# Performance work log

Hardware: AMD Instinct MI355X
Metric: run time of the kernel (lower is better)

Reference implementation:

```python
import jax, jax.numpy as jnp
import numpy as np

ALPHA = 0.2
N_ENT, N_TYP, N_REL, E = 100000, 1000, 200, 500000
D = 64          # nfeat1 = nfeat2 = nhid1 = nhid2 = relation_dim
NHEADS = 2      # forced by the tuple-unpack in the original forward


def _xavier(key, shape):
    fan_out, fan_in = shape[0], shape[-1]
    lim = 1.414 * np.sqrt(6.0 / (fan_in + fan_out))
    return jax.random.uniform(key, shape, jnp.float32, -lim, lim)


def setup_inputs() -> dict:
    key = jax.random.key(0)
    ks = jax.random.split(key, 32)
    inp = {
        "entity_embeddings": jax.random.normal(ks[0], (N_ENT, D), jnp.float32),
        "type_embed": jax.random.normal(ks[1], (N_TYP, D), jnp.float32),
        "relation_embed": jax.random.normal(ks[2], (N_REL, D), jnp.float32),
        "edge_list": jax.random.randint(ks[3], (2, E), 0, N_TYP),  # row0=src entity, row1=dst type; both in-range
        "edge_type": jax.random.randint(ks[4], (E,), 0, N_REL),
        "edge_embed": jax.random.normal(ks[5], (E, D), jnp.float32),
    }
    Din = 3 * D  # cat(x1[src], x2[dst], edge_embed)
    i = 6
    for h in range(NHEADS):
        inp[f"a_e{h}"] = _xavier(ks[i], (D, Din)); i += 1   # entity-side attention proj
        inp[f"v_e{h}"] = _xavier(ks[i], (1, D))[0]; i += 1  # entity-side score vector
        inp[f"a_t{h}"] = _xavier(ks[i], (D, Din)); i += 1   # type-side attention proj
        inp[f"v_t{h}"] = _xavier(ks[i], (1, D))[0]; i += 1
    Ho = NHEADS * D       # 128
    Dout = 3 * Ho         # out layer input cat dim
    inp["a_eo"] = _xavier(ks[i], (Ho, Dout)); i += 1
    inp["v_eo"] = _xavier(ks[i], (1, Ho))[0]; i += 1
    inp["a_to"] = _xavier(ks[i], (Ho, Dout)); i += 1
    inp["v_to"] = _xavier(ks[i], (1, Ho))[0]; i += 1
    inp["W"] = _xavier(ks[i], (D, Ho))  # relation_dim -> nheads*nhid1
    return inp


def _gat_e2t(x1, x2, src, dst, e, a_e, v_e, a_t, v_t, concat):
    """Bipartite sparse GAT layer (KBGAT-style, e2t variant).
    Message m = a @ cat(x1[src], x2[dst], edge_embed); score = exp(-leaky_relu(v . m));
    softmax-normalized scatter-aggregate to entity nodes (by src) and type nodes (by dst)."""
    d1, d2 = x1.shape[1], x2.shape[1]

    def agg(a, v, seg, nseg):
        a1, a2, a3 = a[:, :d1], a[:, d1:d1 + d2], a[:, d1 + d2:]
        # project nodes first, then gather (avoids materializing [E, 3d] cat)
        m = (x1 @ a1.T)[src] + (x2 @ a2.T)[dst] + e @ a3.T     # [E, h]
        s = jnp.exp(-jax.nn.leaky_relu(m @ v, ALPHA))          # [E] unnormalized attention
        num = jax.ops.segment_sum(m * s[:, None], seg, num_segments=nseg)
        den = jax.ops.segment_sum(s, seg, num_segments=nseg)
        h = num / jnp.where(den == 0, 1.0, den)[:, None]
        return jax.nn.elu(h) if concat else h

    h_e = agg(a_e, v_e, src, x1.shape[0])
    h_t = agg(a_t, v_t, dst, x2.shape[0])
    return h_e, h_t


def reference(entity_embeddings, type_embed, relation_embed, edge_list, edge_type, edge_embed,
              a_e0, v_e0, a_t0, v_t0, a_e1, v_e1, a_t1, v_t1,
              a_eo, v_eo, a_to, v_to, W):
    src, dst = edge_list[0], edge_list[1]
    # two attention heads (concat=True -> elu inside)
    h0e, h0t = _gat_e2t(entity_embeddings, type_embed, src, dst, edge_embed, a_e0, v_e0, a_t0, v_t0, True)
    h1e, h1t = _gat_e2t(entity_embeddings, type_embed, src, dst, edge_embed, a_e1, v_e1, a_t1, v_t1, True)
    x1 = jnp.concatenate([h0e, h1e], axis=1)  # [N_ENT, 2*nhid1]
    x2 = jnp.concatenate([h0t, h1t], axis=1)  # [N_TYP, 2*nhid2]
    # dropout is identity at inference
    out_rel = relation_embed @ W              # [N_REL, nheads*nhid1]
    e2 = out_rel[edge_type]                   # per-edge relation embedding
    o1, o2 = _gat_e2t(x1, x2, src, dst, e2, a_eo, v_eo, a_to, v_to, False)
    return jax.nn.elu(o1), jax.nn.elu(o2), out_rel
```

## Files before the change

### kernel.cpp

```cpp
#include <hip/hip_runtime.h>

#define ALPHA 0.2f
#define NT 1000
#define NRELC 200
#define NE 500000
#define N_ENT 100000
#define CH 2048
#define G 245

static constexpr size_t I_STARTS_SRC = 0;
static constexpr size_t I_STARTS_DST = 1001;
static constexpr size_t I_COLSUM     = 2002;
static constexpr size_t I_HIST2      = 4002;
static constexpr size_t I_BASE2      = 494002;
static constexpr size_t I_AB_SRC     = 984002;
static constexpr size_t I_AB_DST     = 1984002;

static constexpr size_t F_U1 = 2984004;
static constexpr size_t F_U2 = F_U1 + 768;
static constexpr size_t F_L1 = F_U2 + 768;
static constexpr size_t F_X1 = F_L1 + 4*130000;
static constexpr size_t F_X2 = F_X1 + 128000;
static constexpr size_t F_OR = F_X2 + 128000;
static constexpr size_t F_L2 = F_OR + 25600;
static constexpr size_t S2F = 283800;
static constexpr size_t WS_FLOATS = F_L2 + 2*S2F;

static constexpr size_t OUT_O2  = 12800000;
static constexpr size_t OUT_REL = 12928000;

__device__ __forceinline__ float eluf(float x) { return x > 0.f ? x : expm1f(x); }
__device__ __forceinline__ float scoref(float slin) {
  return expf(slin > 0.f ? -slin : -ALPHA * slin);
}

__global__ __launch_bounds__(256) void k_hist2(const int* __restrict__ src,
                                               const int* __restrict__ dst,
                                               int* __restrict__ ip) {
  __shared__ int h[NT];
  int bid = blockIdx.x;
  int side = bid >= G;
  int blk = bid - side * G;
  const int* keys = side ? dst : src;
  int j0 = blk * CH;
  int n = min(CH, NE - j0);
  for (int i = threadIdx.x; i < NT; i += 256) h[i] = 0;
  __syncthreads();
  for (int k = threadIdx.x; k < n; k += 256) atomicAdd(&h[keys[j0 + k]], 1);
  __syncthreads();
  int* row = ip + I_HIST2 + (size_t)(side * G + blk) * NT;
  for (int b = threadIdx.x; b < NT; b += 256) row[b] = h[b];
}

__global__ void k_colsum(int* __restrict__ ip) {
  int t = blockIdx.x * 256 + threadIdx.x;
  if (t >= 2 * NT) return;
  int side = t / NT, bin = t - side * NT;
  int s = 0;
  for (int blk = 0; blk < G; ++blk)
    s += ip[I_HIST2 + (size_t)(side * G + blk) * NT + bin];
  ip[I_COLSUM + t] = s;
}

__global__ void k_scan2b(int* __restrict__ ip) {
  __shared__ int buf[1024];
  int t = threadIdx.x;
  for (int side = 0; side < 2; ++side) {
    int v = (t < NT) ? ip[I_COLSUM + side * NT + t] : 0;
    buf[t] = v;
    __syncthreads();
    for (int off = 1; off < 1024; off <<= 1) {
      int x = (t >= off) ? buf[t - off] : 0;
      __syncthreads();
      buf[t] += x;
      __syncthreads();
    }
    int* st = ip + (side ? I_STARTS_DST : I_STARTS_SRC);
    if (t < NT) st[t] = buf[t] - v;
    if (t == NT - 1) st[NT] = buf[t];
    __syncthreads();
  }
}

__global__ void k_bases(int* __restrict__ ip) {
  int t = blockIdx.x * 256 + threadIdx.x;
  if (t >= 2 * NT) return;
  int side = t / NT, bin = t - side * NT;
  int run = ip[(side ? I_STARTS_DST : I_STARTS_SRC) + bin];
  for (int blk = 0; blk < G; ++blk) {
    size_t idx = I_HIST2 + (size_t)(side * G + blk) * NT + bin;
    int c = ip[idx];
    ip[idx + (I_BASE2 - I_HIST2)] = run;
    run += c;
  }
}

__global__ __launch_bounds__(256) void k_binscat(const int* __restrict__ src,
                                                 const int* __restrict__ dst,
                                                 const int* __restrict__ et,
                                                 int* __restrict__ ip) {
  __shared__ int2 bufs[CH];
  __shared__ int loff[1024];
  __shared__ int lcur[1024];
  __shared__ int gbase[1024];
  __shared__ int psum[256];
  int bid = blockIdx.x;
  int side = bid >= G;
  int blk = bid - side * G;
  const int* keys = side ? dst : src;
  const int* oths = side ? src : dst;
  int j0 = blk * CH;
  int n = min(CH, NE - j0);
  int t = threadIdx.x;

  for (int i = t; i < 1024; i += 256) lcur[i] = 0;
  __syncthreads();
  for (int k = t; k < n; k += 256) atomicAdd(&lcur[keys[j0 + k]], 1);
  __syncthreads();
  int c0 = lcur[4*t], c1 = lcur[4*t+1], c2 = lcur[4*t+2], c3 = lcur[4*t+3];
  int s = c0 + c1 + c2 + c3;
  psum[t] = s;
  __syncthreads();
  for (int off = 1; off < 256; off <<= 1) {
    int x = (t >= off) ? psum[t - off] : 0;
    __syncthreads();
    psum[t] += x;
    __syncthreads();
  }
  int base = psum[t] - s;
  loff[4*t]   = base;
  loff[4*t+1] = base + c0;
  loff[4*t+2] = base + c0 + c1;
  loff[4*t+3] = base + c0 + c1 + c2;
  lcur[4*t]   = loff[4*t];
  lcur[4*t+1] = loff[4*t+1];
  lcur[4*t+2] = loff[4*t+2];
  lcur[4*t+3] = loff[4*t+3];
  const int* brow = ip + I_BASE2 + (size_t)(side * G + blk) * NT;
  for (int b = t; b < NT; b += 256) gbase[b] = brow[b];
  __syncthreads();
  for (int k = t; k < n; k += 256) {
    int j = j0 + k;
    int b = keys[j];
    int pos = atomicAdd(&lcur[b], 1);
    bufs[pos] = make_int2(j | (b << 19), oths[j] | (et[j] << 16));
  }
  __syncthreads();
  int2* out = reinterpret_cast<int2*>(ip + (side ? I_AB_DST : I_AB_SRC));
  for (int k = t; k < n; k += 256) {
    int2 q = bufs[k];
    int b = q.x >> 19;
    int posg = gbase[b] + (k - loff[b]);
    out[posg] = make_int2(q.x & 0x7FFFF, q.y);
  }
}

__global__ void k_prep_u(const float* aE0, const float* vE0, const float* aT0, const float* vT0,
                         const float* aE1, const float* vE1, const float* aT1, const float* vT1,
                         const float* aEo, const float* vEo, const float* aTo, const float* vTo,
                         float* ws) {
  int t = blockIdx.x * blockDim.x + threadIdx.x;
  if (t < 768) {
    int c = t / 192, rem = t - c*192;
    int p = rem >> 6, k = rem & 63;
    const float* a = (c==0)?aE0:(c==1)?aT0:(c==2)?aE1:aT1;
    const float* v = (c==0)?vE0:(c==1)?vT0:(c==2)?vE1:vT1;
    float s = 0.f;
    for (int o = 0; o < 64; ++o) s += a[o*192 + p*64 + k] * v[o];
    ws[F_U1 + (size_t)(c*3+p)*64 + k] = s;
  } else if (t < 1536) {
    int tt = t - 768;
    int c = tt / 384, rem = tt - c*384;
    int p = rem >> 7, k = rem & 127;
    const float* a = c ? aTo : aEo;
    const float* v = c ? vTo : vEo;
    float s = 0.f;
    for (int o = 0; o < 128; ++o) s += a[o*384 + p*128 + k] * v[o];
    ws[F_U2 + (size_t)(c*3+p)*128 + k] = s;
  }
}

__global__ __launch_bounds__(256) void k_l1_proj(const float* Ent, const float* Typ,
                                                 const float* aE0, const float* aT0,
                                                 const float* aE1, const float* aT1,
                                                 float* ws) {
  int bid = blockIdx.x;
  int t = threadIdx.x;
  if (bid < 504) {
    __shared__ float xs[16][64];
    int c = bid / 126, rem = bid - c*126;
    int table = rem / 63, tile = rem - table*63;
    int i0 = tile * 16;
    const float* a = (c==0)?aE0:(c==1)?aT0:(c==2)?aE1:aT1;
    const float* x = table ? Typ : Ent;
    float* outb = ws + F_L1 + (size_t)c*130000 + (table ? 64000 : 0);
    for (int idx = t; idx < 1024; idx += 256) {
      int r = idx >> 6, k = idx & 63;
      int i = i0 + r;
      xs[r][k] = (i < NT) ? x[(size_t)i*64 + k] : 0.f;
    }
    __syncthreads();
    int o = t & 63, grp = t >> 6;
    const float* arow = a + o*192 + table*64;
    float acc0 = 0.f, acc1 = 0.f, acc2 = 0.f, acc3 = 0.f;
    #pragma unroll 8
    for (int k = 0; k < 64; ++k) {
      float av = arow[k];
      acc0 += xs[grp*4+0][k] * av;
      acc1 += xs[grp*4+1][k] * av;
      acc2 += xs[grp*4+2][k] * av;
      acc3 += xs[grp*4+3][k] * av;
    }
    int ib = i0 + grp*4;
    if (ib + 0 < NT) outb[(size_t)(ib+0)*64 + o] = acc0;
    if (ib + 1 < NT) outb[(size_t)(ib+1)*64 + o] = acc1;
    if (ib + 2 < NT) outb[(size_t)(ib+2)*64 + o] = acc2;
    if (ib + 3 < NT) outb[(size_t)(ib+3)*64 + o] = acc3;
  } else {
    int idx = (bid - 504) * 256 + t;
    if (idx >= 8000) return;
    int c = idx / 2000, rem = idx - c*2000;
    float* base = ws + F_L1 + (size_t)c * 130000;
    if (rem < 1000) {
      const float* x = Ent + (size_t)rem*64;
      const float* u = ws + F_U1 + (size_t)(c*3)*64;
      float s = 0.f;
      #pragma unroll
      for (int k = 0; k < 64; ++k) s += x[k]*u[k];
      base[128000 + rem] = s;
    } else {
      int i = rem - 1000;
      const float* x = Typ + (size_t)i*64;
      const float* u = ws + F_U1 + (size_t)(c*3+1)*64;
      float s = 0.f;
      #pragma unroll
      for (int k = 0; k < 64; ++k) s += x[k]*u[k];
      base[129000 + i] = s;
    }
  }
}

__global__ __launch_bounds__(256) void k_l1_acc(const float* __restrict__ Eemb,
                                                const float* aE0, const float* aT0,
                                                const float* aE1, const float* aT1,
                                                const int* __restrict__ ip,
                                                float* __restrict__ ws) {
  __shared__ float smem[4434];
  float* TlB   = smem;
  float* cOth0 = smem + 2000;
  float* cOth1 = smem + 3000;
  float* accRf = smem + 2000;
  float* accEf = smem + 4048;
  float* redf  = smem + 4176;
  float* denf  = smem + 4432;

  int side = blockIdx.x >= NT;
  int g = blockIdx.x - side * NT;
  int t = threadIdx.x;
  int sub = t & 15, slot = t >> 4;
  int c0 = side, c1 = side + 2;

  size_t othOff = side ? 128000 : 129000;
  size_t ownOff = side ? 129000 : 128000;
  for (int i = t; i < NT; i += 256) {
    TlB[i] = 0.f; TlB[1000 + i] = 0.f;
    cOth0[i] = ws[F_L1 + (size_t)c0*130000 + othOff + i];
    cOth1[i] = ws[F_L1 + (size_t)c1*130000 + othOff + i];
  }
  if (t < 2) denf[t] = 0.f;
  float ownA = ws[F_L1 + (size_t)c0*130000 + ownOff + g];
  float ownB = ws[F_L1 + (size_t)c1*130000 + ownOff + g];
  float4 w3A = reinterpret_cast<const float4*>(ws + F_U1 + (size_t)(c0*3+2)*64)[sub];
  float4 w3B = reinterpret_cast<const float4*>(ws + F_U1 + (size_t)(c1*3+2)*64)[sub];
  __syncthreads();

  int start = ip[(side ? I_STARTS_DST : I_STARTS_SRC) + g];
  int end   = ip[(side ? I_STARTS_DST : I_STARTS_SRC) + g + 1];
  const int2* ab = reinterpret_cast<const int2*>(ip + (side ? I_AB_DST : I_AB_SRC));
  const float4* EV = reinterpret_cast<const float4*>(Eemb);

  float4 acc0 = make_float4(0.f,0.f,0.f,0.f);
  float4 acc1 = make_float4(0.f,0.f,0.f,0.f);
  float d0 = 0.f, d1 = 0.f;

  int p = start + slot;
  for (; p + 48 < end; p += 64) {
    int2 q0 = ab[p], q1 = ab[p+16], q2 = ab[p+32], q3 = ab[p+48];
    float4 e0 = EV[(size_t)q0.x*16 + sub];
    float4 e1 = EV[(size_t)q1.x*16 + sub];
    float4 e2 = EV[(size_t)q2.x*16 + sub];
    float4 e3 = EV[(size_t)q3.x*16 + sub];
    float rA0 = e0.x*w3A.x + e0.y*w3A.y + e0.z*w3A.z + e0.w*w3A.w;
    float rB0 = e0.x*w3B.x + e0.y*w3B.y + e0.z*w3B.z + e0.w*w3B.w;
    float rA1 = e1.x*w3A.x + e1.y*w3A.y + e1.z*w3A.z + e1.w*w3A.w;
    float rB1 = e1.x*w3B.x + e1.y*w3B.y + e1.z*w3B.z + e1.w*w3B.w;
    float rA2 = e2.x*w3A.x + e2.y*w3A.y + e2.z*w3A.z + e2.w*w3A.w;
    float rB2 = e2.x*w3B.x + e2.y*w3B.y + e2.z*w3B.z + e2.w*w3B.w;
    float rA3 = e3.x*w3A.x + e3.y*w3A.y + e3.z*w3A.z + e3.w*w3A.w;
    float rB3 = e3.x*w3B.x + e3.y*w3B.y + e3.z*w3B.z + e3.w*w3B.w;
    #pragma unroll
    for (int sh = 1; sh < 16; sh <<= 1) {
      rA0 += __shfl_xor(rA0, sh, 16); rB0 += __shfl_xor(rB0, sh, 16);
      rA1 += __shfl_xor(rA1, sh, 16); rB1 += __shfl_xor(rB1, sh, 16);
      rA2 += __shfl_xor(rA2, sh, 16); rB2 += __shfl_xor(rB2, sh, 16);
      rA3 += __shfl_xor(rA3, sh, 16); rB3 += __shfl_xor(rB3, sh, 16);
    }
    int o0 = q0.y & 0xFFFF, o1 = q1.y & 0xFFFF, o2 = q2.y & 0xFFFF, o3 = q3.y & 0xFFFF;
    float sA0 = scoref(ownA + cOth0[o0] + rA0);
    float sB0 = scoref(ownB + cOth1[o0] + rB0);
    float sA1 = scoref(ownA + cOth0[o1] + rA1);
    float sB1 = scoref(ownB + cOth1[o1] + rB1);
    float sA2 = scoref(ownA + cOth0[o2] + rA2);
    float sB2 = scoref(ownB + cOth1[o2] + rB2);
    float sA3 = scoref(ownA + cOth0[o3] + rA3);
    float sB3 = scoref(ownB + cOth1[o3] + rB3);
    acc0.x += sA0*e0.x + sA1*e1.x + sA2*e2.x + sA3*e3.x;
    acc0.y += sA0*e0.y + sA1*e1.y + sA2*e2.y + sA3*e3.y;
    acc0.z += sA0*e0.z + sA1*e1.z + sA2*e2.z + sA3*e3.z;
    acc0.w += sA0*e0.w + sA1*e1.w + sA2*e2.w + sA3*e3.w;
    acc1.x += sB0*e0.x + sB1*e1.x + sB2*e2.x + sB3*e3.x;
    acc1.y += sB0*e0.y + sB1*e1.y + sB2*e2.y + sB3*e3.y;
    acc1.z += sB0*e0.z + sB1*e1.z + sB2*e2.z + sB3*e3.z;
    acc1.w += sB0*e0.w + sB1*e1.w + sB2*e2.w + sB3*e3.w;
    if (sub == 0) {
      atomicAdd(&TlB[o0], sA0); atomicAdd(&TlB[1000+o0], sB0);
      atomicAdd(&TlB[o1], sA1); atomicAdd(&TlB[1000+o1], sB1);
      atomicAdd(&TlB[o2], sA2); atomicAdd(&TlB[1000+o2], sB2);
      atomicAdd(&TlB[o3], sA3); atomicAdd(&TlB[1000+o3], sB3);
      d0 += sA0 + sA1 + sA2 + sA3;
      d1 += sB0 + sB1 + sB2 + sB3;
    }
  }
  for (; p < end; p += 16) {
    int2 q = ab[p];
    float4 ev = EV[(size_t)q.x*16 + sub];
    float rA = ev.x*w3A.x + ev.y*w3A.y + ev.z*w3A.z + ev.w*w3A.w;
    float rB = ev.x*w3B.x + ev.y*w3B.y + ev.z*w3B.z + ev.w*w3B.w;
    #pragma unroll
    for (int sh = 1; sh < 16; sh <<= 1) {
      rA += __shfl_xor(rA, sh, 16);
      rB += __shfl_xor(rB, sh, 16);
    }
    int oth = q.y & 0xFFFF;
    float sA = scoref(ownA + cOth0[oth] + rA);
    float sB = scoref(ownB + cOth1[oth] + rB);
    acc0.x += sA*ev.x; acc0.y += sA*ev.y; acc0.z += sA*ev.z; acc0.w += sA*ev.w;
    acc1.x += sB*ev.x; acc1.y += sB*ev.y; acc1.z += sB*ev.z; acc1.w += sB*ev.w;
    if (sub == 0) {
      atomicAdd(&TlB[oth], sA);
      atomicAdd(&TlB[1000+oth], sB);
      d0 += sA; d1 += sB;
    }
  }
  __syncthreads();
  *reinterpret_cast<float4*>(&accRf[slot*64 + sub*4])        = acc0;
  *reinterpret_cast<float4*>(&accRf[1024 + slot*64 + sub*4]) = acc1;
  if (sub == 0) { atomicAdd(&denf[0], d0); atomicAdd(&denf[1], d1); }
  __syncthreads();
  if (t < 128) {
    int ci = t >> 6, o = t & 63;
    float s = 0.f;
    #pragma unroll
    for (int sl = 0; sl < 16; ++sl) s += accRf[ci*1024 + sl*64 + o];
    accEf[ci*64 + o] = s;
  }
  __syncthreads();

  int o = t & 63, part = t >> 6;
  size_t othPOff = side ? 0 : 64000;
  size_t ownPOff = side ? 64000 : 0;
  #pragma unroll
  for (int ci = 0; ci < 2; ++ci) {
    int c = side + 2*ci;
    const float* Pc = ws + F_L1 + (size_t)c * 130000;
    const float* Poth = Pc + othPOff;
    float sum = 0.f;
    for (int dd = part*250; dd < part*250 + 250; ++dd)
      sum += TlB[ci*1000 + dd] * Poth[(size_t)dd*64 + o];
    redf[t] = sum;
    __syncthreads();
    if (part == 0) {
      sum = redf[o] + redf[64+o] + redf[128+o] + redf[192+o];
      const float* a = (c==0)?aE0:(c==1)?aT0:(c==2)?aE1:aT1;
      const float* a3 = a + o*192 + 128;
      float acc = 0.f;
      #pragma unroll
      for (int k = 0; k < 64; ++k) acc += accEf[ci*64 + k]*a3[k];
      float den = denf[ci];
      float own = Pc[ownPOff + (size_t)g*64 + o];
      float num = sum + acc + den*own;
      float h = num / (den == 0.f ? 1.f : den);
      float* dst = ws + (side ? F_X2 : F_X1);
      dst[(size_t)g*128 + ci*64 + o] = eluf(h);
    }
    __syncthreads();
  }
}

__global__ void k_relW(const float* Rel, const float* W, float* ws, float* dout) {
  int t = blockIdx.x * blockDim.x + threadIdx.x;
  if (t >= NRELC*128) return;
  int r = t >> 7, o = t & 127;
  const float* x = Rel + (size_t)r*64;
  float s = 0.f;
  #pragma unroll
  for (int k = 0; k < 64; ++k) s += x[k] * W[(size_t)k*128 + o];
  ws[F_OR + t] = s;
  dout[OUT_REL + t] = s;
}

__global__ __launch_bounds__(256) void k_l2_proj(const float* aEo, const float* aTo,
                                                 float* ws) {
  int bid = blockIdx.x;
  int t = threadIdx.x;
  const float* x1 = ws + F_X1;
  const float* x2 = ws + F_X2;
  const float* orel = ws + F_OR;
  if (bid < 278) {
    __shared__ float xs[16][128];
    int c = bid / 139, rem = bid - c*139;
    const float* a = c ? aTo : aEo;
    float* cb = ws + F_L2 + (size_t)c * S2F;
    const float* x; int part, tile, nrows; float* outb;
    if (rem < 63)       { x = x1;   part = 0; tile = rem;       nrows = NT;    outb = cb; }
    else if (rem < 126) { x = x2;   part = 1; tile = rem - 63;  nrows = NT;    outb = cb + 128000; }
    else                { x = orel; part = 2; tile = rem - 126; nrows = NRELC; outb = cb + 256000; }
    int i0 = tile * 16;
    for (int idx = t; idx < 2048; idx += 256) {
      int r = idx >> 7, k = idx & 127;
      int i = i0 + r;
      xs[r][k] = (i < nrows) ? x[(size_t)i*128 + k] : 0.f;
    }
    __syncthreads();
    int o = t & 127, grp = t >> 7;
    const float* arow = a + (size_t)o*384 + part*128;
    float acc[8] = {0.f,0.f,0.f,0.f,0.f,0.f,0.f,0.f};
    #pragma unroll 4
    for (int k = 0; k < 128; ++k) {
      float av = arow[k];
      #pragma unroll
      for (int r = 0; r < 8; ++r)
        acc[r] += xs[grp*8+r][k] * av;
    }
    int ib = i0 + grp*8;
    #pragma unroll
    for (int r = 0; r < 8; ++r)
      if (ib + r < nrows) outb[(size_t)(ib+r)*128 + o] = acc[r];
  } else {
    int idx = (bid - 278) * 256 + t;
    if (idx >= 4400) return;
    int c = idx / 2200, rem = idx - c*2200;
    float* base = ws + F_L2 + (size_t)c * S2F;
    if (rem < 1000) {
      const float* u = ws + F_U2 + (size_t)(c*3)*128;
      const float* x = x1 + (size_t)rem*128;
      float s = 0.f;
      for (int k = 0; k < 128; ++k) s += x[k]*u[k];
      base[281600 + rem] = s;
    } else if (rem < 2000) {
      int i = rem - 1000;
      const float* u = ws + F_U2 + (size_t)(c*3+1)*128;
      const float* x = x2 + (size_t)i*128;
      float s = 0.f;
      for (int k = 0; k < 128; ++k) s += x[k]*u[k];
      base[282600 + i] = s;
    } else {
      int r = rem - 2000;
      const float* u = ws + F_U2 + (size_t)(c*3+2)*128;
      const float* x = orel + (size_t)r*128;
      float s = 0.f;
      for (int k = 0; k < 128; ++k) s += x[k]*u[k];
      base[283600 + r] = s;
    }
  }
}

__global__ __launch_bounds__(256) void k_l2_seg(const int* __restrict__ ip,
                                                float* __restrict__ ws,
                                                float* __restrict__ dout) {
  __shared__ float Tl[2][NT];
  __shared__ float Ul[2][NRELC];
  __shared__ float cOthL[NT];
  __shared__ float cRelL[NRELC];
  __shared__ float red[2][256];
  __shared__ float denl[2];

  int c = blockIdx.x >= 500;
  int gp = blockIdx.x - c * 500;
  int g0 = gp * 2;
  int t = threadIdx.x;
  float* base = ws + F_L2 + (size_t)c * S2F;

  size_t othOff = c ? 281600 : 282600;
  size_t ownOff = c ? 282600 : 281600;
  for (int i = t; i < NT; i += 256) { Tl[0][i] = 0.f; Tl[1][i] = 0.f; cOthL[i] = base[othOff + i]; }
  for (int i = t; i < NRELC; i += 256) { Ul[0][i] = 0.f; Ul[1][i] = 0.f; cRelL[i] = base[283600 + i]; }
  if (t < 2) denl[t] = 0.f;
  float own0 = base[ownOff + g0];
  float own1 = base[ownOff + g0 + 1];
  __syncthreads();

  const int* st = ip + (c ? I_STARTS_DST : I_STARTS_SRC);
  int s0 = st[g0], split = st[g0 + 1], e1 = st[g0 + 2];
  const int2* ab = reinterpret_cast<const int2*>(ip + (c ? I_AB_DST : I_AB_SRC));

  float d0 = 0.f, d1 = 0.f;
  for (int p = s0 + t; p < e1; p += 256) {
    int2 q = ab[p];
    int oth = q.y & 0xFFFF;
    int r = q.y >> 16;
    int ls = p >= split;
    float sv = scoref((ls ? own1 : own0) + cOthL[oth] + cRelL[r]);
    atomicAdd(&Tl[ls][oth], sv);
    atomicAdd(&Ul[ls][r], sv);
    if (ls) d1 += sv; else d0 += sv;
  }
  atomicAdd(&denl[0], d0);
  atomicAdd(&denl[1], d1);
  __syncthreads();

  int o = t & 127, part = t >> 7;
  const float* Qoth = base + (c ? 0 : 128000);
  const float* R3 = base + 256000;
  float sum0 = 0.f, sum1 = 0.f;
  for (int dd = part*500; dd < part*500 + 500; ++dd) {
    float qv = Qoth[(size_t)dd*128 + o];
    sum0 += Tl[0][dd] * qv;
    sum1 += Tl[1][dd] * qv;
  }
  for (int rr = part*100; rr < part*100 + 100; ++rr) {
    float qv = R3[(size_t)rr*128 + o];
    sum0 += Ul[0][rr] * qv;
    sum1 += Ul[1][rr] * qv;
  }
  red[0][t] = sum0;
  red[1][t] = sum1;
  __syncthreads();
  int li = part;
  float den = denl[li];
  float sum = red[li][o] + red[li][128 + o];
  int gw = g0 + li;
  float ownQ = base[(c ? 128000 : 0) + (size_t)gw*128 + o];
  float num = sum + den * ownQ;
  float h = num / (den == 0.f ? 1.f : den);
  size_t off = c ? (OUT_O2 + (size_t)gw*128 + o) : ((size_t)gw*128 + o);
  dout[off] = eluf(h);
}

extern "C" void kernel_launch(void* const* d_in, const int* in_sizes, int n_in,
                              void* d_out, int out_size, void* d_ws, size_t ws_size,
                              hipStream_t stream) {
  (void)in_sizes; (void)n_in;
  const float* Ent = (const float*)d_in[0];
  const float* Typ = (const float*)d_in[1];
  const float* Rel = (const float*)d_in[2];
  const int*   edge = (const int*)d_in[3];
  const int*   etyp = (const int*)d_in[4];
  const float* Eemb = (const float*)d_in[5];
  const float* aE0 = (const float*)d_in[6];
  const float* vE0 = (const float*)d_in[7];
  const float* aT0 = (const float*)d_in[8];
  const float* vT0 = (const float*)d_in[9];
  const float* aE1 = (const float*)d_in[10];
  const float* vE1 = (const float*)d_in[11];
  const float* aT1 = (const float*)d_in[12];
  const float* vT1 = (const float*)d_in[13];
  const float* aEo = (const float*)d_in[14];
  const float* vEo = (const float*)d_in[15];
  const float* aTo = (const float*)d_in[16];
  const float* vTo = (const float*)d_in[17];
  const float* W   = (const float*)d_in[18];
  float* ws  = (float*)d_ws;
  int*   ip  = (int*)d_ws;
  float* out = (float*)d_out;
  const int* srcA = edge;
  const int* dstA = edge + NE;

  if (ws_size < WS_FLOATS * sizeof(float)) return;

  hipMemsetAsync(d_out, 0, (size_t)out_size * sizeof(float), stream);

  k_hist2  <<<2*G, 256, 0, stream>>>(srcA, dstA, ip);
  k_colsum <<<8, 256, 0, stream>>>(ip);
  k_scan2b <<<1, 1024, 0, stream>>>(ip);
  k_bases  <<<8, 256, 0, stream>>>(ip);
  k_binscat<<<2*G, 256, 0, stream>>>(srcA, dstA, etyp, ip);
  k_prep_u <<<6, 256, 0, stream>>>(aE0,vE0,aT0,vT0,aE1,vE1,aT1,vT1,aEo,vEo,aTo,vTo,ws);
  k_l1_proj<<<536, 256, 0, stream>>>(Ent, Typ, aE0, aT0, aE1, aT1, ws);
  k_l1_acc <<<2000, 256, 0, stream>>>(Eemb, aE0, aT0, aE1, aT1, ip, ws);
  k_relW   <<<100, 256, 0, stream>>>(Rel, W, ws, out);
  k_l2_proj<<<296, 256, 0, stream>>>(aEo, aTo, ws);
  k_l2_seg <<<1000, 256, 0, stream>>>(ip, ws, out);
}
```

Measured before the change: 253.1 us.

## Embed per-edge other-side score terms in binned edge records

The edge binning kernel now runs after the layer-1 projections and writes 16-byte records that also carry the two precomputed other-side score contributions. The layer-1 accumulate kernel then reads these from the record instead of staging 1000-entry tables in shared memory. Its accumulator reduction is split into two passes so the shared-memory footprint shrinks, which may raise occupancy. In exchange, the edge-record arrays double in size, so layer 2, which also reads them, moves more bytes per edge.

```diff
diff --git a/kernel.cpp b/kernel.cpp
--- a/kernel.cpp
+++ b/kernel.cpp
@@ -13,10 +13,10 @@
 static constexpr size_t I_COLSUM     = 2002;
 static constexpr size_t I_HIST2      = 4002;
 static constexpr size_t I_BASE2      = 494002;
-static constexpr size_t I_AB_SRC     = 984002;
-static constexpr size_t I_AB_DST     = 1984002;
-
-static constexpr size_t F_U1 = 2984004;
+static constexpr size_t I_AB_SRC     = 984004;
+static constexpr size_t I_AB_DST     = 2984004;
+
+static constexpr size_t F_U1 = 4984004;
 static constexpr size_t F_U2 = F_U1 + 768;
 static constexpr size_t F_L1 = F_U2 + 768;
 static constexpr size_t F_X1 = F_L1 + 4*130000;
@@ -92,66 +92,6 @@
     int c = ip[idx];
     ip[idx + (I_BASE2 - I_HIST2)] = run;
     run += c;
-  }
-}
-
-__global__ __launch_bounds__(256) void k_binscat(const int* __restrict__ src,
-                                                 const int* __restrict__ dst,
-                                                 const int* __restrict__ et,
-                                                 int* __restrict__ ip) {
-  __shared__ int2 bufs[CH];
-  __shared__ int loff[1024];
-  __shared__ int lcur[1024];
-  __shared__ int gbase[1024];
-  __shared__ int psum[256];
-  int bid = blockIdx.x;
-  int side = bid >= G;
-  int blk = bid - side * G;
-  const int* keys = side ? dst : src;
-  const int* oths = side ? src : dst;
-  int j0 = blk * CH;
-  int n = min(CH, NE - j0);
-  int t = threadIdx.x;
-
-  for (int i = t; i < 1024; i += 256) lcur[i] = 0;
-  __syncthreads();
-  for (int k = t; k < n; k += 256) atomicAdd(&lcur[keys[j0 + k]], 1);
-  __syncthreads();
-  int c0 = lcur[4*t], c1 = lcur[4*t+1], c2 = lcur[4*t+2], c3 = lcur[4*t+3];
-  int s = c0 + c1 + c2 + c3;
-  psum[t] = s;
-  __syncthreads();
-  for (int off = 1; off < 256; off <<= 1) {
-    int x = (t >= off) ? psum[t - off] : 0;
-    __syncthreads();
-    psum[t] += x;
-    __syncthreads();
-  }
-  int base = psum[t] - s;
-  loff[4*t]   = base;
-  loff[4*t+1] = base + c0;
-  loff[4*t+2] = base + c0 + c1;
-  loff[4*t+3] = base + c0 + c1 + c2;
-  lcur[4*t]   = loff[4*t];
-  lcur[4*t+1] = loff[4*t+1];
-  lcur[4*t+2] = loff[4*t+2];
-  lcur[4*t+3] = loff[4*t+3];
-  const int* brow = ip + I_BASE2 + (size_t)(side * G + blk) * NT;
-  for (int b = t; b < NT; b += 256) gbase[b] = brow[b];
-  __syncthreads();
-  for (int k = t; k < n; k += 256) {
-    int j = j0 + k;
-    int b = keys[j];
-    int pos = atomicAdd(&lcur[b], 1);
-    bufs[pos] = make_int2(j | (b << 19), oths[j] | (et[j] << 16));
-  }
-  __syncthreads();
-  int2* out = reinterpret_cast<int2*>(ip + (side ? I_AB_DST : I_AB_SRC));
-  for (int k = t; k < n; k += 256) {
-    int2 q = bufs[k];
-    int b = q.x >> 19;
-    int posg = gbase[b] + (k - loff[b]);
-    out[posg] = make_int2(q.x & 0x7FFFF, q.y);
   }
 }
 
@@ -240,19 +180,83 @@
   }
 }
 
+__global__ __launch_bounds__(256) void k_binscat(const int* __restrict__ src,
+                                                 const int* __restrict__ dst,
+                                                 const int* __restrict__ et,
+                                                 int* __restrict__ ip,
+                                                 const float* __restrict__ ws) {
+  __shared__ int2 bufs[CH];
+  __shared__ int loff[1024];
+  __shared__ int lcur[1024];
+  __shared__ int gbase[1024];
+  __shared__ int psum[256];
+  int bid = blockIdx.x;
+  int side = bid >= G;
+  int blk = bid - side * G;
+  const int* keys = side ? dst : src;
+  const int* oths = side ? src : dst;
+  int j0 = blk * CH;
+  int n = min(CH, NE - j0);
+  int t = threadIdx.x;
+
+  for (int i = t; i < 1024; i += 256) lcur[i] = 0;
+  __syncthreads();
+  for (int k = t; k < n; k += 256) atomicAdd(&lcur[keys[j0 + k]], 1);
+  __syncthreads();
+  int c0 = lcur[4*t], c1 = lcur[4*t+1], c2 = lcur[4*t+2], c3 = lcur[4*t+3];
+  int s = c0 + c1 + c2 + c3;
+  psum[t] = s;
+  __syncthreads();
+  for (int off = 1; off < 256; off <<= 1) {
+    int x = (t >= off) ? psum[t - off] : 0;
+    __syncthreads();
+    psum[t] += x;
+    __syncthreads();
+  }
+  int base = psum[t] - s;
+  loff[4*t]   = base;
+  loff[4*t+1] = base + c0;
+  loff[4*t+2] = base + c0 + c1;
+  loff[4*t+3] = base + c0 + c1 + c2;
+  lcur[4*t]   = loff[4*t];
+  lcur[4*t+1] = loff[4*t+1];
+  lcur[4*t+2] = loff[4*t+2];
+  lcur[4*t+3] = loff[4*t+3];
+  const int* brow = ip + I_BASE2 + (size_t)(side * G + blk) * NT;
+  for (int b = t; b < NT; b += 256) gbase[b] = brow[b];
+  __syncthreads();
+  for (int k = t; k < n; k += 256) {
+    int j = j0 + k;
+    int b = keys[j];
+    int pos = atomicAdd(&lcur[b], 1);
+    bufs[pos] = make_int2(j | (b << 19), oths[j] | (et[j] << 16));
+  }
+  __syncthreads();
+  size_t othOff = side ? 128000 : 129000;
+  const float* cT0 = ws + F_L1 + (size_t)(side    )*130000 + othOff;
+  const float* cT1 = ws + F_L1 + (size_t)(side + 2)*130000 + othOff;
+  int4* out4 = reinterpret_cast<int4*>(ip + (side ? I_AB_DST : I_AB_SRC));
+  for (int k = t; k < n; k += 256) {
+    int2 q = bufs[k];
+    int b = q.x >> 19;
+    int posg = gbase[b] + (k - loff[b]);
+    int oth = q.y & 0xFFFF;
+    out4[posg] = make_int4(q.x & 0x7FFFF, q.y,
+                           __float_as_int(cT0[oth]), __float_as_int(cT1[oth]));
+  }
+}
+
 __global__ __launch_bounds__(256) void k_l1_acc(const float* __restrict__ Eemb,
                                                 const float* aE0, const float* aT0,
                                                 const float* aE1, const float* aT1,
                                                 const int* __restrict__ ip,
                                                 float* __restrict__ ws) {
-  __shared__ float smem[4434];
+  __shared__ float smem[3154];
   float* TlB   = smem;
-  float* cOth0 = smem + 2000;
-  float* cOth1 = smem + 3000;
   float* accRf = smem + 2000;
-  float* accEf = smem + 4048;
-  float* redf  = smem + 4176;
-  float* denf  = smem + 4432;
+  float* accEf = smem + 3024;
+  float* denf  = smem + 3152;
+  float* redf  = smem + 2000;
 
   int side = blockIdx.x >= NT;
   int g = blockIdx.x - side * NT;
@@ -260,13 +264,8 @@
   int sub = t & 15, slot = t >> 4;
   int c0 = side, c1 = side + 2;
 
-  size_t othOff = side ? 128000 : 129000;
   size_t ownOff = side ? 129000 : 128000;
-  for (int i = t; i < NT; i += 256) {
-    TlB[i] = 0.f; TlB[1000 + i] = 0.f;
-    cOth0[i] = ws[F_L1 + (size_t)c0*130000 + othOff + i];
-    cOth1[i] = ws[F_L1 + (size_t)c1*130000 + othOff + i];
-  }
+  for (int i = t; i < NT; i += 256) { TlB[i] = 0.f; TlB[1000 + i] = 0.f; }
   if (t < 2) denf[t] = 0.f;
   float ownA = ws[F_L1 + (size_t)c0*130000 + ownOff + g];
   float ownB = ws[F_L1 + (size_t)c1*130000 + ownOff + g];
@@ -276,7 +275,7 @@
 
   int start = ip[(side ? I_STARTS_DST : I_STARTS_SRC) + g];
   int end   = ip[(side ? I_STARTS_DST : I_STARTS_SRC) + g + 1];
-  const int2* ab = reinterpret_cast<const int2*>(ip + (side ? I_AB_DST : I_AB_SRC));
+  const int4* ab = reinterpret_cast<const int4*>(ip + (side ? I_AB_DST : I_AB_SRC));
   const float4* EV = reinterpret_cast<const float4*>(Eemb);
 
   float4 acc0 = make_float4(0.f,0.f,0.f,0.f);
@@ -285,7 +284,7 @@
 
   int p = start + slot;
   for (; p + 48 < end; p += 64) {
-    int2 q0 = ab[p], q1 = ab[p+16], q2 = ab[p+32], q3 = ab[p+48];
+    int4 q0 = ab[p], q1 = ab[p+16], q2 = ab[p+32], q3 = ab[p+48];
     float4 e0 = EV[(size_t)q0.x*16 + sub];
     float4 e1 = EV[(size_t)q1.x*16 + sub];
     float4 e2 = EV[(size_t)q2.x*16 + sub];
@@ -306,14 +305,14 @@
       rA3 += __shfl_xor(rA3, sh, 16); rB3 += __shfl_xor(rB3, sh, 16);
     }
     int o0 = q0.y & 0xFFFF, o1 = q1.y & 0xFFFF, o2 = q2.y & 0xFFFF, o3 = q3.y & 0xFFFF;
-    float sA0 = scoref(ownA + cOth0[o0] + rA0);
-    float sB0 = scoref(ownB + cOth1[o0] + rB0);
-    float sA1 = scoref(ownA + cOth0[o1] + rA1);
-    float sB1 = scoref(ownB + cOth1[o1] + rB1);
-    float sA2 = scoref(ownA + cOth0[o2] + rA2);
-    float sB2 = scoref(ownB + cOth1[o2] + rB2);
-    float sA3 = scoref(ownA + cOth0[o3] + rA3);
-    float sB3 = scoref(ownB + cOth1[o3] + rB3);
+    float sA0 = scoref(ownA + __int_as_float(q0.z) + rA0);
+    float sB0 = scoref(ownB + __int_as_float(q0.w) + rB0);
+    float sA1 = scoref(ownA + __int_as_float(q1.z) + rA1);
+    float sB1 = scoref(ownB + __int_as_float(q1.w) + rB1);
+    float sA2 = scoref(ownA + __int_as_float(q2.z) + rA2);
+    float sB2 = scoref(ownB + __int_as_float(q2.w) + rB2);
+    float sA3 = scoref(ownA + __int_as_float(q3.z) + rA3);
+    float sB3 = scoref(ownB + __int_as_float(q3.w) + rB3);
     acc0.x += sA0*e0.x + sA1*e1.x + sA2*e2.x + sA3*e3.x;
     acc0.y += sA0*e0.y + sA1*e1.y + sA2*e2.y + sA3*e3.y;
     acc0.z += sA0*e0.z + sA1*e1.z + sA2*e2.z + sA3*e3.z;
@@ -332,7 +331,7 @@
     }
   }
   for (; p < end; p += 16) {
-    int2 q = ab[p];
+    int4 q = ab[p];
     float4 ev = EV[(size_t)q.x*16 + sub];
     float rA = ev.x*w3A.x + ev.y*w3A.y + ev.z*w3A.z + ev.w*w3A.w;
     float rB = ev.x*w3B.x + ev.y*w3B.y + ev.z*w3B.z + ev.w*w3B.w;
@@ -342,8 +341,8 @@
       rB += __shfl_xor(rB, sh, 16);
     }
     int oth = q.y & 0xFFFF;
-    float sA = scoref(ownA + cOth0[oth] + rA);
-    float sB = scoref(ownB + cOth1[oth] + rB);
+    float sA = scoref(ownA + __int_as_float(q.z) + rA);
+    float sB = scoref(ownB + __int_as_float(q.w) + rB);
     acc0.x += sA*ev.x; acc0.y += sA*ev.y; acc0.z += sA*ev.z; acc0.w += sA*ev.w;
     acc1.x += sB*ev.x; acc1.y += sB*ev.y; acc1.z += sB*ev.z; acc1.w += sB*ev.w;
     if (sub == 0) {
@@ -352,17 +351,24 @@
       d0 += sA; d1 += sB;
     }
   }
-  __syncthreads();
-  *reinterpret_cast<float4*>(&accRf[slot*64 + sub*4])        = acc0;
-  *reinterpret_cast<float4*>(&accRf[1024 + slot*64 + sub*4]) = acc1;
   if (sub == 0) { atomicAdd(&denf[0], d0); atomicAdd(&denf[1], d1); }
   __syncthreads();
-  if (t < 128) {
-    int ci = t >> 6, o = t & 63;
+  *reinterpret_cast<float4*>(&accRf[slot*64 + sub*4]) = acc0;
+  __syncthreads();
+  if (t < 64) {
     float s = 0.f;
     #pragma unroll
-    for (int sl = 0; sl < 16; ++sl) s += accRf[ci*1024 + sl*64 + o];
-    accEf[ci*64 + o] = s;
+    for (int sl = 0; sl < 16; ++sl) s += accRf[sl*64 + t];
+    accEf[t] = s;
+  }
+  __syncthreads();
+  *reinterpret_cast<float4*>(&accRf[slot*64 + sub*4]) = acc1;
+  __syncthreads();
+  if (t < 64) {
+    float s = 0.f;
+    #pragma unroll
+    for (int sl = 0; sl < 16; ++sl) s += accRf[sl*64 + t];
+    accEf[64 + t] = s;
   }
   __syncthreads();
 
@@ -502,11 +508,11 @@
 
   const int* st = ip + (c ? I_STARTS_DST : I_STARTS_SRC);
   int s0 = st[g0], split = st[g0 + 1], e1 = st[g0 + 2];
-  const int2* ab = reinterpret_cast<const int2*>(ip + (c ? I_AB_DST : I_AB_SRC));
+  const int4* ab = reinterpret_cast<const int4*>(ip + (c ? I_AB_DST : I_AB_SRC));
 
   float d0 = 0.f, d1 = 0.f;
   for (int p = s0 + t; p < e1; p += 256) {
-    int2 q = ab[p];
+    int4 q = ab[p];
     int oth = q.y & 0xFFFF;
     int r = q.y >> 16;
     int ls = p >= split;
@@ -584,9 +590,9 @@
   k_colsum <<<8, 256, 0, stream>>>(ip);
   k_scan2b <<<1, 1024, 0, stream>>>(ip);
   k_bases  <<<8, 256, 0, stream>>>(ip);
-  k_binscat<<<2*G, 256, 0, stream>>>(srcA, dstA, etyp, ip);
   k_prep_u <<<6, 256, 0, stream>>>(aE0,vE0,aT0,vT0,aE1,vE1,aT1,vT1,aEo,vEo,aTo,vTo,ws);
   k_l1_proj<<<536, 256, 0, stream>>>(Ent, Typ, aE0, aT0, aE1, aT1, ws);
+  k_binscat<<<2*G, 256, 0, stream>>>(srcA, dstA, etyp, ip, ws);
   k_l1_acc <<<2000, 256, 0, stream>>>(Eemb, aE0, aT0, aE1, aT1, ip, ws);
   k_relW   <<<100, 256, 0, stream>>>(Rel, W, ws, out);
   k_l2_proj<<<296, 256, 0, stream>>>(aEo, aTo, ws);
```

Measured after the change: 256.3 us. About the same (+1.2%).
